# Kernel tuning notes

Measured on AMD Instinct MI355X. Metric: run time of the kernel, lower is better.

Reference implementation:

```python
import jax, jax.numpy as jnp
import numpy as np

# ---- config (matches init_kwargs) ----
B, N = 2, 192
NCG, L0, L1, ANUM = 16, 16, 8, 2
RAD_MAXR, NB, H = 4.0, 10, 32
SQ2 = 1.4142135623730951

RS0 = {0: NCG}
RS_HID = {0: L0, 1: L1}
RS_FIN = {0: ANUM, 1: ANUM}
LMAX_SH = 2


def relu_r(x):  # rescaled_act.relu: unit second moment under N(0,1)
    return jax.nn.relu(x) * SQ2


def sigmoid_r(x):  # rescaled_act.sigmoid
    return jax.nn.sigmoid(x) * 1.84623


def _cg():
    # Real-basis coupling tensors C[i_out, j_in, m_filter]; l=1 components ordered (y,z,x).
    c000 = np.ones((1, 1, 1))
    eye3 = np.eye(3)
    c101 = (eye3 / np.sqrt(3.0)).reshape(3, 1, 3)
    c011 = (eye3 / np.sqrt(3.0)).reshape(1, 3, 3)
    c110 = (eye3 / np.sqrt(3.0)).reshape(3, 3, 1)
    eps = np.zeros((3, 3, 3))
    for i, j, k in [(0, 1, 2), (1, 2, 0), (2, 0, 1)]:
        eps[i, j, k] = 1.0
        eps[j, i, k] = -1.0
    c111 = eps / np.sqrt(6.0)
    c = 1.0925484305920792
    b = 0.31539156525252005
    d = 0.5462742152960396
    m = np.zeros((3, 3, 5))  # index 0=y, 1=z, 2=x
    m[2, 0, 0] = m[0, 2, 0] = c / 2            # ~ x*y
    m[0, 1, 1] = m[1, 0, 1] = c / 2            # ~ y*z
    m[1, 1, 2] = 2 * b; m[0, 0, 2] = -b; m[2, 2, 2] = -b  # ~ 2z^2-x^2-y^2
    m[2, 1, 3] = m[1, 2, 3] = c / 2            # ~ x*z
    m[2, 2, 4] = d; m[0, 0, 4] = -d            # ~ x^2-y^2
    c112 = m / np.linalg.norm(m)
    return {(0, 0, 0): c000, (1, 0, 1): c101, (0, 1, 1): c011,
            (1, 1, 0): c110, (1, 1, 1): c111, (1, 1, 2): c112}

CG = {k: jnp.asarray(v, jnp.float32) for k, v in _cg().items()}


def paths_for(rs_in, rs_out):
    out = []
    for lo in sorted(rs_out):
        for li in sorted(rs_in):
            for lf in range(abs(lo - li), min(lo + li, LMAX_SH) + 1):
                out.append((lo, li, lf, rs_out[lo], rs_in[li]))
    return out


def total_w(rs_in, rs_out):
    return sum(mo * mi for _, _, _, mo, mi in paths_for(rs_in, rs_out))


def convolution(feat, geo, w0, b0, wout, rs_in, rs_out):
    # feat: dict l -> [B,N,mul,2l+1]; geo: [B,N,3]
    rel = geo[:, :, None, :] - geo[:, None, :, :]              # [B,N,N,3]
    r = jnp.sqrt(jnp.sum(rel * rel, -1) + 1e-12)               # [B,N,N]
    u = rel / jnp.maximum(r, 1e-6)[..., None]
    x_, y_, z_ = u[..., 0], u[..., 1], u[..., 2]
    Y = {0: jnp.full(r.shape + (1,), 0.28209479177387814, r.dtype),
         1: 0.4886025119029199 * jnp.stack([y_, z_, x_], -1),
         2: jnp.stack([1.0925484305920792 * x_ * y_,
                       1.0925484305920792 * y_ * z_,
                       0.31539156525252005 * (2 * z_ * z_ - x_ * x_ - y_ * y_),
                       1.0925484305920792 * x_ * z_,
                       0.5462742152960396 * (x_ * x_ - y_ * y_)], -1)}
    # CosineBasisModel: overlapping cos^2 bumps on [0, RAD_MAXR]
    centers = jnp.linspace(0.0, RAD_MAXR, NB)
    step = RAD_MAXR / (NB - 1)
    dg = (r[..., None] - centers) / step
    basis = jnp.where(jnp.abs(dg) < 1.0, jnp.cos(0.5 * jnp.pi * dg) ** 2, 0.0)
    h = relu_r(basis @ (w0 / np.sqrt(NB)) + b0)                # [B,N,N,H]
    Rw = h @ (wout / np.sqrt(H))                               # [B,N,N,total_w]

    plist = paths_for(rs_in, rs_out)
    npaths = {lo: sum(1 for p in plist if p[0] == lo) for lo in rs_out}
    out = {lo: jnp.zeros(geo.shape[:2] + (rs_out[lo], 2 * lo + 1), geo.dtype)
           for lo in rs_out}
    off = 0
    for lo, li, lf, mo, mi in plist:
        w = Rw[..., off:off + mo * mi].reshape(Rw.shape[:3] + (mo, mi))
        off += mo * mi
        contrib = jnp.einsum('zabuv,zabm,ijm,zbvj->zaui', w, Y[lf],
                             CG[(lo, li, lf)], feat[li], optimize=True)
        out[lo] = out[lo] + contrib / np.sqrt(mi * npaths[lo])
    return out


def gated_block(feat, geo, w0, b0, wout, rs_in, rs_out):
    n_gates = sum(m for l, m in rs_out.items() if l > 0)
    rs_conv = dict(rs_out)
    rs_conv[0] = rs_out.get(0, 0) + n_gates
    c = convolution(feat, geo, w0, b0, wout, rs_in, rs_conv)
    m0 = rs_out.get(0, 0)
    out = {0: relu_r(c[0][:, :, :m0])}
    gates = sigmoid_r(c[0][:, :, m0:])                         # [B,N,n_gates,1]
    g_off = 0
    for l in sorted(rs_out):
        if l == 0:
            continue
        ml = rs_out[l]
        out[l] = c[l] * gates[:, :, g_off:g_off + ml]
        g_off += ml
    return out


def _forward(features, geometry, c0_w0, c0_b0, c0_wout, c1_w0, c1_b0, c1_wout,
             c2_w0, c2_b0, c2_wout):
    s = 1.0 / np.sqrt(N)  # output.div(geometry.size(1)**0.5) before every layer
    f = {0: features[..., None] * s}
    f = gated_block(f, geometry, c0_w0, c0_b0, c0_wout, RS0, RS_HID)
    f = {l: v * s for l, v in f.items()}
    f = gated_block(f, geometry, c1_w0, c1_b0, c1_wout, RS_HID, RS_HID)
    f = {l: v * s for l, v in f.items()}
    f = convolution(f, geometry, c2_w0, c2_b0, c2_wout, RS_HID, RS_FIN)
    # final Rs = [(1,0),(1,1)] * atomic_nums -> interleave scalar+vector per species
    out = jnp.concatenate([f[0], f[1]], axis=-1)               # [B,N,ANUM,4]
    return out.reshape(B, N, ANUM * 4)


def setup_inputs() -> dict:
    key = jax.random.key(0)
    ks = jax.random.split(key, 8)
    RS_G = {0: L0 + L1, 1: L1}  # gated conv output: scalars + gates, then l=1
    return {
        'features': jax.random.normal(ks[0], (B, N, NCG), jnp.float32),
        'geometry': jax.random.normal(ks[1], (B, N, 3), jnp.float32),
        'c0_w0': jax.random.normal(ks[2], (NB, H), jnp.float32),
        'c0_b0': jnp.zeros((H,), jnp.float32),
        'c0_wout': jax.random.normal(ks[3], (H, total_w(RS0, RS_G)), jnp.float32),
        'c1_w0': jax.random.normal(ks[4], (NB, H), jnp.float32),
        'c1_b0': jnp.zeros((H,), jnp.float32),
        'c1_wout': jax.random.normal(ks[5], (H, total_w(RS_HID, RS_G)), jnp.float32),
        'c2_w0': jax.random.normal(ks[6], (NB, H), jnp.float32),
        'c2_b0': jnp.zeros((H,), jnp.float32),
        'c2_wout': jax.random.normal(ks[7], (H, total_w(RS_HID, RS_FIN)), jnp.float32),
    }


def reference(features, geometry, c0_w0, c0_b0, c0_wout, c1_w0, c1_b0, c1_wout,
              c2_w0, c2_b0, c2_wout):
    return _forward(features, geometry, c0_w0, c0_b0, c0_wout,
                    c1_w0, c1_b0, c1_wout, c2_w0, c2_b0, c2_wout)
```

## Files before the change

### kernel.cpp

```cpp
#include <hip/hip_runtime.h>
#include <math.h>


#define NN 192
#define BB 2
#define SPLIT 8
#define NS 24
#define NBASIS 10
#define HHID 32

__device__ __forceinline__ float relu_r(float x) {
    return fmaxf(x, 0.0f) * 1.4142135623730951f;
}
__device__ __forceinline__ float sigmoid_r(float x) {
    return (1.0f / (1.0f + expf(-x))) * 1.84623f;
}
__device__ __forceinline__ float dot4(float4 a, float4 b) {
    return a.x * b.x + a.y * b.y + a.z * b.z + a.w * b.w;
}

#define S_SCALE 0.07216878364870323f
#define ISQ10   0.31622776601683794f
#define I32     0.1767766952966369f

__global__ __launch_bounds__(256) void tfn_act(
    const float* __restrict__ part, float* __restrict__ fa0, float* __restrict__ fa1)
{
    int t = blockIdx.x * 256 + threadIdx.x;
    if (t >= BB * NN * 40) return;
    int atom = t / 40, c = t - atom * 40;
    const float* p = &part[atom * SPLIT * 48];
    if (c < 16) {
        float s = 0.0f;
#pragma unroll
        for (int sp = 0; sp < SPLIT; ++sp) s += p[sp * 48 + c];
        fa0[atom * 16 + c] = relu_r(s) * S_SCALE;
    } else {
        int j = c - 16, u = j & 7;
        float g = 0.0f, v = 0.0f;
#pragma unroll
        for (int sp = 0; sp < SPLIT; ++sp) {
            g += p[sp * 48 + 16 + u];
            v += p[sp * 48 + 24 + j];
        }
        fa1[atom * 24 + j] = v * sigmoid_r(g) * S_SCALE;
    }
}

template <int LAYER>
__global__ __launch_bounds__(256, 4) void tfn_s1(
    const float* __restrict__ fin0,
    const float* __restrict__ fin1,
    const float* __restrict__ geo,
    const float* __restrict__ w0g,
    const float* __restrict__ b0g,
    const float* __restrict__ wout,
    float* __restrict__ part)
{
    constexpr int TC    = (LAYER == 0) ? 64 : 144;
    constexpr int TSTR  = (LAYER == 0) ? 64 : 168;
    constexpr int TW    = (LAYER == 0) ? 512 : (LAYER == 1 ? 896 : 128);
    constexpr int NOUT  = (LAYER == 2) ? 8 : 48;
    constexpr int MSTRE = (LAYER == 0) ? 68 : 148;
    constexpr int R     = (LAYER == 0) ? 2 : 4;
    constexpr int C     = (LAYER == 0) ? 4 : 5;

    constexpr int oT   = 0;
    constexpr int oF0  = oT + NS * TSTR;
    constexpr int oF1  = oF0 + NS * 16;
    constexpr int oY   = oF1 + ((LAYER == 0) ? 0 : NS * 24);
    constexpr int oBas = oY + NS * 8;
    constexpr int oH   = oBas + NS * NBASIS;
    constexpr int SM0  = oH + NS * HHID;
    constexpr int oU   = 32 * MSTRE;
    constexpr int SMe  = oU + NOUT * 33;
    constexpr int SM   = (SM0 > SMe) ? SM0 : SMe;
    __shared__ float sm[SM];

    const int tid  = threadIdx.x;
    const int blk  = blockIdx.x;
    const int sp   = blk & (SPLIT - 1);
    const int atom = blk >> 3;
    const int z    = atom / NN, a = atom % NN;
    const int nb0  = sp * NS;

    if constexpr (LAYER == 0) {
        for (int i = tid; i < NS * 16; i += 256)
            sm[oF0 + i] = fin0[(z * NN + nb0) * 16 + i] * S_SCALE;
    } else {
        for (int i = tid; i < NS * 16; i += 256)
            sm[oF0 + i] = fin0[(z * NN + nb0) * 16 + i];
        for (int i = tid; i < NS * 24; i += 256)
            sm[oF1 + i] = fin1[(z * NN + nb0) * 24 + i];
    }
    {
        const float ax = geo[(z * NN + a) * 3 + 0];
        const float ay = geo[(z * NN + a) * 3 + 1];
        const float az = geo[(z * NN + a) * 3 + 2];
        for (int idx = tid; idx < NS * 12; idx += 256) {
            int bl = idx / 12, it = idx - bl * 12;
            const float* gb = &geo[(z * NN + nb0 + bl) * 3];
            float rx = ax - gb[0], ry = ay - gb[1], rz = az - gb[2];
            float r = sqrtf(rx * rx + ry * ry + rz * rz + 1e-12f);
            if (it < NBASIS) {
                float dg = r * 2.25f - (float)it;
                float bas = 0.0f;
                if (fabsf(dg) < 1.0f) {
                    float cc = cosf(1.5707963267948966f * dg);
                    bas = cc * cc;
                }
                sm[oBas + bl * NBASIS + it] = bas;
            } else {
                float inv = 1.0f / fmaxf(r, 1e-6f);
                float ux = rx * inv, uy = ry * inv, uz = rz * inv;
                if (it == 10) {
                    sm[oY + bl * 8 + 0] = 0.4886025119029199f * uy;
                    sm[oY + bl * 8 + 1] = 0.4886025119029199f * uz;
                    sm[oY + bl * 8 + 2] = 0.4886025119029199f * ux;
                } else {
                    sm[oY + bl * 8 + 3] = 1.0925484305920792f * ux * uy;
                    sm[oY + bl * 8 + 4] = 1.0925484305920792f * uy * uz;
                    sm[oY + bl * 8 + 5] = 0.31539156525252005f * (2.0f * uz * uz - ux * ux - uy * uy);
                    sm[oY + bl * 8 + 6] = 1.0925484305920792f * ux * uz;
                    sm[oY + bl * 8 + 7] = 0.5462742152960396f * (ux * ux - uy * uy);
                }
            }
        }
    }
    __syncthreads();

    for (int idx = tid; idx < NS * 32; idx += 256) {
        int bl = idx >> 5, j = idx & 31;
        float su = 0.0f;
#pragma unroll
        for (int k = 0; k < NBASIS; ++k)
            su += sm[oBas + bl * NBASIS + k] * w0g[k * HHID + j];
        sm[oH + idx] = relu_r(su * ISQ10 + b0g[j]);
    }
    if constexpr (LAYER == 0) {
        for (int idx = tid; idx < NS * 16; idx += 256) {
            int loc = idx >> 4, c = idx & 15;
            sm[oT + loc * TSTR + c] = 0.28209479177387814f * sm[oF0 + loc * 16 + c];
        }
#pragma unroll
        for (int i2 = 0; i2 < 3; ++i2)
            for (int idx = tid; idx < NS * 16; idx += 256) {
                int loc = idx >> 4, v = idx & 15;
                sm[oT + loc * TSTR + 16 + i2 * 16 + v] =
                    sm[oY + loc * 8 + i2] * sm[oF0 + loc * 16 + v] * 0.5773502691896258f;
            }
    } else {
        for (int idx = tid; idx < NS * 16; idx += 256) {
            int loc = idx >> 4, c = idx & 15;
            sm[oT + loc * TSTR + c] = 0.28209479177387814f * sm[oF0 + loc * 16 + c];
        }
        for (int idx = tid; idx < NS * 8; idx += 256) {
            int loc = idx >> 3, u = idx & 7;
            const float* Yb = &sm[oY + loc * 8];
            const float* fT = &sm[oF1 + loc * 24];
            sm[oT + loc * TSTR + 16 + u] =
                (fT[u] * Yb[0] + fT[8 + u] * Yb[1] + fT[16 + u] * Yb[2]) * 0.5773502691896258f;
        }
#pragma unroll
        for (int i2 = 0; i2 < 3; ++i2)
            for (int idx = tid; idx < NS * 16; idx += 256) {
                int loc = idx >> 4, v = idx & 15;
                sm[oT + loc * TSTR + 24 + i2 * 16 + v] =
                    sm[oY + loc * 8 + i2] * sm[oF0 + loc * 16 + v] * 0.5773502691896258f;
            }
        for (int idx = tid; idx < NS * 24; idx += 256) {
            int loc = idx / 24, j = idx - loc * 24;
            sm[oT + loc * TSTR + 72 + j] =
                sm[oF1 + loc * 24 + j] * (0.28209479177387814f * 0.5773502691896258f);
        }
#pragma unroll
        for (int i2 = 0; i2 < 3; ++i2) {
            const int i1 = (i2 + 1) % 3, i3 = (i2 + 2) % 3;
            for (int idx = tid; idx < NS * 8; idx += 256) {
                int loc = idx >> 3, u = idx & 7;
                const float* Yb = &sm[oY + loc * 8];
                const float* fT = &sm[oF1 + loc * 24];
                sm[oT + loc * TSTR + 96 + i2 * 8 + u] =
                    (fT[i1 * 8 + u] * Yb[i3] - fT[i3 * 8 + u] * Yb[i1]) * 0.4082482904638631f;
            }
        }
#pragma unroll
        for (int i2 = 0; i2 < 3; ++i2)
            for (int idx = tid; idx < NS * 8; idx += 256) {
                int loc = idx >> 3, u = idx & 7;
                const float* Yb = &sm[oY + loc * 8];
                const float* fT = &sm[oF1 + loc * 24];
                const float D  = 0.31622776601683794f;
                const float Bc = 0.18257418583505536f;
                float f0v = fT[u], f1v = fT[8 + u], f2v = fT[16 + u];
                float Y20 = Yb[3], Y21 = Yb[4], Y22 = Yb[5], Y23 = Yb[6], Y24 = Yb[7];
                float val;
                if (i2 == 0)      val = D * (Y20 * f2v + Y21 * f1v) - (Bc * Y22 + D * Y24) * f0v;
                else if (i2 == 1) val = D * (Y21 * f0v + Y23 * f2v) + 2.0f * Bc * Y22 * f1v;
                else              val = D * (Y20 * f0v + Y23 * f1v + Y24 * f2v) - Bc * Y22 * f2v;
                sm[oT + loc * TSTR + 120 + i2 * 8 + u] = val;
            }
    }
    __syncthreads();

    float acc[R][C];
#pragma unroll
    for (int rr = 0; rr < R; ++rr)
#pragma unroll
        for (int cc = 0; cc < C; ++cc) acc[rr][cc] = 0.0f;

    if constexpr (LAYER == 0) {
        const int hr = tid >> 4, cg = tid & 15;
#pragma unroll 4
        for (int bl = 0; bl < NS; ++bl) {
            float2 hv = *(const float2*)&sm[oH + bl * 32 + hr * 2];
            float4 tv = *(const float4*)&sm[oT + bl * 64 + cg * 4];
            float hvv[2] = {hv.x, hv.y};
            float tvv[4] = {tv.x, tv.y, tv.z, tv.w};
#pragma unroll
            for (int rr = 0; rr < 2; ++rr)
#pragma unroll
                for (int cc = 0; cc < 4; ++cc) acc[rr][cc] += hvv[rr] * tvv[cc];
        }
    } else {
        const int hr = tid >> 5, cg = tid & 31;
#pragma unroll 4
        for (int bl = 0; bl < NS; ++bl) {
            float4 hv = *(const float4*)&sm[oH + bl * 32 + hr * 4];
            const float* tp = &sm[oT + bl * TSTR + cg * 5];
            float hvv[4] = {hv.x, hv.y, hv.z, hv.w};
            float t0 = tp[0], t1 = tp[1], t2 = tp[2], t3 = tp[3], t4 = tp[4];
#pragma unroll
            for (int rr = 0; rr < 4; ++rr) {
                acc[rr][0] += hvv[rr] * t0;
                acc[rr][1] += hvv[rr] * t1;
                acc[rr][2] += hvv[rr] * t2;
                acc[rr][3] += hvv[rr] * t3;
                acc[rr][4] += hvv[rr] * t4;
            }
        }
    }
    __syncthreads();

    {
        const int hr = (LAYER == 0) ? (tid >> 4) : (tid >> 5);
        const int cg = (LAYER == 0) ? (tid & 15) : (tid & 31);
#pragma unroll
        for (int rr = 0; rr < R; ++rr)
#pragma unroll
            for (int cc = 0; cc < C; ++cc) {
                int col = cg * C + cc;
                if (col < TC) sm[(hr * R + rr) * MSTRE + col] = acc[rr][cc];
            }
    }
    __syncthreads();

    constexpr int NITEM = NOUT * 32;
    for (int rp = 0; rp < NITEM / 256; ++rp) {
        int idx = rp * 256 + tid;
        int h = idx / NOUT, o = idx - h * NOUT;
        const float* wr = &wout[h * TW];
        const float* mr = &sm[h * MSTRE];
        float U;
        if constexpr (LAYER == 0) {
            const float sc = I32 * 0.25f;
            float accv;
            if (o < 24) {
                const float4* w4 = (const float4*)(wr + o * 16);
                const float4* m4 = (const float4*)(mr);
                accv = dot4(w4[0], m4[0]) + dot4(w4[1], m4[1])
                     + dot4(w4[2], m4[2]) + dot4(w4[3], m4[3]);
            } else {
                int j = o - 24, u = j & 7, i2 = j >> 3;
                const float4* w4 = (const float4*)(wr + 384 + u * 16);
                const float4* m4 = (const float4*)(mr + 16 + i2 * 16);
                accv = dot4(w4[0], m4[0]) + dot4(w4[1], m4[1])
                     + dot4(w4[2], m4[2]) + dot4(w4[3], m4[3]);
            }
            U = accv * sc;
        } else if constexpr (LAYER == 1) {
            float aA, aB;
            if (o < 24) {
                const float4* w4 = (const float4*)(wr + o * 16);
                const float4* m4 = (const float4*)(mr);
                aA = dot4(w4[0], m4[0]) + dot4(w4[1], m4[1])
                   + dot4(w4[2], m4[2]) + dot4(w4[3], m4[3]);
                const float4* w8 = (const float4*)(wr + 384 + o * 8);
                const float4* m8 = (const float4*)(mr + 16);
                aB = dot4(w8[0], m8[0]) + dot4(w8[1], m8[1]);
                U = (aA * I32 + aB * 0.25f) * I32;
            } else {
                int j = o - 24, u = j & 7, i2 = j >> 3;
                const float4* w4 = (const float4*)(wr + 576 + u * 16);
                const float4* m4 = (const float4*)(mr + 24 + i2 * 16);
                aA = dot4(w4[0], m4[0]) + dot4(w4[1], m4[1])
                   + dot4(w4[2], m4[2]) + dot4(w4[3], m4[3]);
                const float4* wB0 = (const float4*)(wr + 704 + u * 8);
                const float4* wB1 = (const float4*)(wr + 768 + u * 8);
                const float4* wB2 = (const float4*)(wr + 832 + u * 8);
                const float4* mB0 = (const float4*)(mr + 72 + i2 * 8);
                const float4* mB1 = (const float4*)(mr + 96 + i2 * 8);
                const float4* mB2 = (const float4*)(mr + 120 + i2 * 8);
                aB = dot4(wB0[0], mB0[0]) + dot4(wB0[1], mB0[1])
                   + dot4(wB1[0], mB1[0]) + dot4(wB1[1], mB1[1])
                   + dot4(wB2[0], mB2[0]) + dot4(wB2[1], mB2[1]);
                U = (aA * 0.125f + aB * I32) * I32;
            }
        } else {
            float aA, aB;
            if (o < 2) {
                const float4* w4 = (const float4*)(wr + o * 16);
                const float4* m4 = (const float4*)(mr);
                aA = dot4(w4[0], m4[0]) + dot4(w4[1], m4[1])
                   + dot4(w4[2], m4[2]) + dot4(w4[3], m4[3]);
                const float4* w8 = (const float4*)(wr + 32 + o * 8);
                const float4* m8 = (const float4*)(mr + 16);
                aB = dot4(w8[0], m8[0]) + dot4(w8[1], m8[1]);
                U = (aA * I32 + aB * 0.25f) * I32;
            } else {
                int j = o - 2, u = j & 1, i2 = j >> 1;
                const float4* w4 = (const float4*)(wr + 48 + u * 16);
                const float4* m4 = (const float4*)(mr + 24 + i2 * 16);
                aA = dot4(w4[0], m4[0]) + dot4(w4[1], m4[1])
                   + dot4(w4[2], m4[2]) + dot4(w4[3], m4[3]);
                const float4* wB0 = (const float4*)(wr + 80 + u * 8);
                const float4* wB1 = (const float4*)(wr + 96 + u * 8);
                const float4* wB2 = (const float4*)(wr + 112 + u * 8);
                const float4* mB0 = (const float4*)(mr + 72 + i2 * 8);
                const float4* mB1 = (const float4*)(mr + 96 + i2 * 8);
                const float4* mB2 = (const float4*)(mr + 120 + i2 * 8);
                aB = dot4(wB0[0], mB0[0]) + dot4(wB0[1], mB0[1])
                   + dot4(wB1[0], mB1[0]) + dot4(wB1[1], mB1[1])
                   + dot4(wB2[0], mB2[0]) + dot4(wB2[1], mB2[1]);
                U = (aA * 0.125f + aB * I32) * I32;
            }
        }
        sm[oU + o * 33 + h] = U;
    }
    __syncthreads();

    if (tid < NOUT) {
        float su = 0.0f;
#pragma unroll
        for (int h = 0; h < 32; ++h) su += sm[oU + tid * 33 + h];
        part[blk * NOUT + tid] = su;
    }
}

__global__ __launch_bounds__(256) void tfn_fin(
    const float* __restrict__ part2, float* __restrict__ out)
{
    int t = blockIdx.x * 256 + threadIdx.x;
    int atom = t >> 3, o = t & 7;
    const float* p = &part2[atom * SPLIT * 8];
    float su = ((p[o] + p[8 + o]) + (p[16 + o] + p[24 + o]))
             + ((p[32 + o] + p[40 + o]) + (p[48 + o] + p[56 + o]));
    int pos;
    if (o < 2) pos = o * 4;
    else { int j = o - 2; int i2 = j >> 1, u = j & 1; pos = u * 4 + 1 + i2; }
    out[atom * 8 + pos] = su;
}

template <int LAYER>
__global__ __launch_bounds__(256) void tfn_layer_mono(
    const float* __restrict__ geo,
    const float* __restrict__ fin0,
    const float* __restrict__ fin1,
    const float* __restrict__ w0,
    const float* __restrict__ b0g,
    const float* __restrict__ wout,
    float* __restrict__ o0,
    float* __restrict__ o1)
{
    constexpr int TC   = (LAYER == 0) ? 64 : 144;
    constexpr int TW   = (LAYER == 0) ? 512 : (LAYER == 1 ? 896 : 128);
    constexpr int CPT  = TC / 8;
    constexpr int CPTT = TC / 16;

    const int tid = threadIdx.x;
    const int blk = blockIdx.x;
    const int z = blk / NN, a = blk % NN;

    __shared__ float geoL[NN * 3];
    __shared__ float f0L[NN * 16];
    __shared__ float f1L[(LAYER == 0) ? 1 : (NN * 24)];
    __shared__ float w0L[NBASIS * HHID];
    __shared__ float b0L[HHID];
    __shared__ float YC[16 * 8];
    __shared__ float basC[16 * NBASIS];
    __shared__ float hC[16 * HHID];
    __shared__ float tC[16 * TC];
    __shared__ float Mlds[HHID * TC];
    __shared__ float outS[32];

    const float s = S_SCALE;

    for (int i = tid; i < NN * 3; i += 256) geoL[i] = geo[z * NN * 3 + i];
    for (int i = tid; i < NN * 16; i += 256) {
        float v = fin0[z * NN * 16 + i];
        if (LAYER == 0) v *= s;
        f0L[i] = v;
    }
    if constexpr (LAYER != 0) {
        for (int i = tid; i < NN * 24; i += 256) f1L[i] = fin1[z * NN * 24 + i];
    }
    for (int i = tid; i < NBASIS * HHID; i += 256) w0L[i] = w0[i];
    if (tid < HHID) b0L[tid] = b0g[tid];
    __syncthreads();

    const float ax = geoL[a * 3 + 0], ay = geoL[a * 3 + 1], az = geoL[a * 3 + 2];

    float Macc[CPT];
#pragma unroll
    for (int j = 0; j < CPT; ++j) Macc[j] = 0.0f;
    const int hh  = tid >> 3;
    const int cg0 = (tid & 7) * CPT;

    for (int cb = 0; cb < NN / 16; ++cb) {
        {
            const int bl = tid & 15, item = tid >> 4;
            const int b = cb * 16 + bl;
            float rx = ax - geoL[b * 3 + 0];
            float ry = ay - geoL[b * 3 + 1];
            float rz = az - geoL[b * 3 + 2];
            float r = sqrtf(rx * rx + ry * ry + rz * rz + 1e-12f);
            float inv = 1.0f / fmaxf(r, 1e-6f);
            float ux = rx * inv, uy = ry * inv, uz = rz * inv;
            if (item < NBASIS) {
                float dg = r * 2.25f - (float)item;
                float bas = 0.0f;
                if (fabsf(dg) < 1.0f) {
                    float cc = cosf(1.5707963267948966f * dg);
                    bas = cc * cc;
                }
                basC[bl * NBASIS + item] = bas;
            } else if (item == 10) {
                YC[bl * 8 + 0] = 0.4886025119029199f * uy;
                YC[bl * 8 + 1] = 0.4886025119029199f * uz;
                YC[bl * 8 + 2] = 0.4886025119029199f * ux;
            } else if (item == 11) {
                YC[bl * 8 + 3] = 1.0925484305920792f * ux * uy;
                YC[bl * 8 + 4] = 1.0925484305920792f * uy * uz;
                YC[bl * 8 + 5] = 0.31539156525252005f * (2.0f * uz * uz - ux * ux - uy * uy);
                YC[bl * 8 + 6] = 1.0925484305920792f * ux * uz;
                YC[bl * 8 + 7] = 0.5462742152960396f * (ux * ux - uy * uy);
            }
        }
        __syncthreads();

#pragma unroll
        for (int rep = 0; rep < 2; ++rep) {
            int idx = tid + rep * 256;
            int bl = idx >> 5, h2 = idx & 31;
            float su = 0.0f;
#pragma unroll
            for (int k = 0; k < NBASIS; ++k) su += basC[bl * NBASIS + k] * w0L[k * HHID + h2];
            hC[bl * HHID + h2] = relu_r(su * ISQ10 + b0L[h2]);
        }

        {
            const int bl = tid >> 4, cg = tid & 15;
            const int b = cb * 16 + bl;
            const float* Yb = &YC[bl * 8];
#pragma unroll
            for (int jj = 0; jj < CPTT; ++jj) {
                int c = cg * CPTT + jj;
                float val;
                if constexpr (LAYER == 0) {
                    if (c < 16) {
                        val = 0.28209479177387814f * f0L[b * 16 + c];
                    } else {
                        int q = c - 16, v = q / 3, i2 = q % 3;
                        val = Yb[i2] * f0L[b * 16 + v] * 0.5773502691896258f;
                    }
                } else {
                    if (c < 16) {
                        val = 0.28209479177387814f * f0L[b * 16 + c];
                    } else if (c < 24) {
                        int v = c - 16;
                        const float* f = &f1L[(b * 8 + v) * 3];
                        val = (f[0] * Yb[0] + f[1] * Yb[1] + f[2] * Yb[2]) * 0.5773502691896258f;
                    } else if (c < 72) {
                        int q = c - 24, v = q / 3, i2 = q % 3;
                        val = Yb[i2] * f0L[b * 16 + v] * 0.5773502691896258f;
                    } else if (c < 96) {
                        int q = c - 72, v = q / 3, i2 = q % 3;
                        val = f1L[(b * 8 + v) * 3 + i2] * (0.28209479177387814f * 0.5773502691896258f);
                    } else if (c < 120) {
                        int q = c - 96, v = q / 3, i2 = q % 3;
                        const float* f = &f1L[(b * 8 + v) * 3];
                        int i1 = (i2 + 1) % 3, i3 = (i2 + 2) % 3;
                        val = (f[i1] * Yb[i3] - f[i3] * Yb[i1]) * 0.4082482904638631f;
                    } else {
                        int q = c - 120, v = q / 3, i2 = q % 3;
                        const float* f = &f1L[(b * 8 + v) * 3];
                        const float D = 0.31622776601683794f;
                        const float Bc = 0.18257418583505536f;
                        float Y20 = Yb[3], Y21 = Yb[4], Y22 = Yb[5], Y23 = Yb[6], Y24 = Yb[7];
                        if (i2 == 0)      val = D * (Y20 * f[2] + Y21 * f[1]) - (Bc * Y22 + D * Y24) * f[0];
                        else if (i2 == 1) val = D * (Y21 * f[0] + Y23 * f[2]) + 2.0f * Bc * Y22 * f[1];
                        else              val = D * (Y20 * f[0] + Y23 * f[1] + Y24 * f[2]) - Bc * Y22 * f[2];
                    }
                }
                tC[bl * TC + c] = val;
            }
        }
        __syncthreads();

#pragma unroll 4
        for (int bl = 0; bl < 16; ++bl) {
            float hv = hC[bl * HHID + hh];
#pragma unroll
            for (int j = 0; j < CPT; ++j) Macc[j] += hv * tC[bl * TC + cg0 + j];
        }
        __syncthreads();
    }

#pragma unroll
    for (int j = 0; j < CPT; ++j) Mlds[hh * TC + cg0 + j] = Macc[j];
    __syncthreads();

    const float i32 = I32;

    if constexpr (LAYER == 0) {
        const float sc = i32 * 0.25f;
        float o1v = 0.0f;
        if (tid < 24) {
            float acc = 0.0f;
            for (int h2 = 0; h2 < 32; ++h2) {
                const float* wr = &wout[h2 * TW + tid * 16];
                const float* mr = &Mlds[h2 * TC];
#pragma unroll
                for (int v = 0; v < 16; ++v) acc += wr[v] * mr[v];
            }
            outS[tid] = acc * sc;
        } else if (tid >= 32 && tid < 56) {
            int idx = tid - 32, u = idx / 3, i2 = idx % 3;
            float acc = 0.0f;
            for (int h2 = 0; h2 < 32; ++h2) {
                const float* wr = &wout[h2 * TW + 384 + u * 16];
                const float* mr = &Mlds[h2 * TC + 16 + i2];
#pragma unroll
                for (int v = 0; v < 16; ++v) acc += wr[v] * mr[v * 3];
            }
            o1v = acc * sc;
        }
        __syncthreads();
        if (tid < 16) {
            o0[(z * NN + a) * 16 + tid] = relu_r(outS[tid]) * s;
        } else if (tid >= 32 && tid < 56) {
            int idx = tid - 32, u = idx / 3, i2 = idx % 3;
            float g = sigmoid_r(outS[16 + u]);
            o1[((z * NN + a) * 8 + u) * 3 + i2] = o1v * g * s;
        }
    } else if constexpr (LAYER == 1) {
        float o1v = 0.0f;
        if (tid < 24) {
            float aA = 0.0f, aB = 0.0f;
            for (int h2 = 0; h2 < 32; ++h2) {
                const float* wr = &wout[h2 * TW];
                const float* mr = &Mlds[h2 * TC];
#pragma unroll
                for (int v = 0; v < 16; ++v) aA += wr[tid * 16 + v] * mr[v];
#pragma unroll
                for (int v = 0; v < 8; ++v) aB += wr[384 + tid * 8 + v] * mr[16 + v];
            }
            outS[tid] = (aA * i32 + aB * 0.25f) * i32;
        } else if (tid >= 32 && tid < 56) {
            int idx = tid - 32, u = idx / 3, i2 = idx % 3;
            float aA = 0.0f, aB = 0.0f;
            for (int h2 = 0; h2 < 32; ++h2) {
                const float* wr = &wout[h2 * TW];
                const float* mr = &Mlds[h2 * TC];
#pragma unroll
                for (int v = 0; v < 16; ++v) aA += wr[576 + u * 16 + v] * mr[24 + v * 3 + i2];
#pragma unroll
                for (int v = 0; v < 8; ++v)
                    aB += wr[704 + u * 8 + v] * mr[72 + v * 3 + i2]
                        + wr[768 + u * 8 + v] * mr[96 + v * 3 + i2]
                        + wr[832 + u * 8 + v] * mr[120 + v * 3 + i2];
            }
            o1v = (aA * 0.125f + aB * i32) * i32;
        }
        __syncthreads();
        if (tid < 16) {
            o0[(z * NN + a) * 16 + tid] = relu_r(outS[tid]) * s;
        } else if (tid >= 32 && tid < 56) {
            int idx = tid - 32, u = idx / 3, i2 = idx % 3;
            float g = sigmoid_r(outS[16 + u]);
            o1[((z * NN + a) * 8 + u) * 3 + i2] = o1v * g * s;
        }
    } else {
        if (tid < 2) {
            float aA = 0.0f, aB = 0.0f;
            for (int h2 = 0; h2 < 32; ++h2) {
                const float* wr = &wout[h2 * TW];
                const float* mr = &Mlds[h2 * TC];
#pragma unroll
                for (int v = 0; v < 16; ++v) aA += wr[tid * 16 + v] * mr[v];
#pragma unroll
                for (int v = 0; v < 8; ++v) aB += wr[32 + tid * 8 + v] * mr[16 + v];
            }
            o0[(z * NN + a) * 8 + tid * 4] = (aA * i32 + aB * 0.25f) * i32;
        } else if (tid >= 32 && tid < 38) {
            int idx = tid - 32, u = idx / 3, i2 = idx % 3;
            float aA = 0.0f, aB = 0.0f;
            for (int h2 = 0; h2 < 32; ++h2) {
                const float* wr = &wout[h2 * TW];
                const float* mr = &Mlds[h2 * TC];
#pragma unroll
                for (int v = 0; v < 16; ++v) aA += wr[48 + u * 16 + v] * mr[24 + v * 3 + i2];
#pragma unroll
                for (int v = 0; v < 8; ++v)
                    aB += wr[80 + u * 8 + v] * mr[72 + v * 3 + i2]
                        + wr[96 + u * 8 + v] * mr[96 + v * 3 + i2]
                        + wr[112 + u * 8 + v] * mr[120 + v * 3 + i2];
            }
            o0[(z * NN + a) * 8 + u * 4 + 1 + i2] = (aA * 0.125f + aB * i32) * i32;
        }
    }
}

extern "C" void kernel_launch(void* const* d_in, const int* in_sizes, int n_in,
                              void* d_out, int out_size, void* d_ws, size_t ws_size,
                              hipStream_t stream) {
    const float* features = (const float*)d_in[0];
    const float* geometry = (const float*)d_in[1];
    const float* c0w0   = (const float*)d_in[2];
    const float* c0b0   = (const float*)d_in[3];
    const float* c0wout = (const float*)d_in[4];
    const float* c1w0   = (const float*)d_in[5];
    const float* c1b0   = (const float*)d_in[6];
    const float* c1wout = (const float*)d_in[7];
    const float* c2w0   = (const float*)d_in[8];
    const float* c2b0   = (const float*)d_in[9];
    const float* c2wout = (const float*)d_in[10];
    float* out = (float*)d_out;

    float* ws = (float*)d_ws;
    const size_t NBLK  = (size_t)BB * NN * SPLIT;
    const size_t NATOM = (size_t)BB * NN;
    const size_t need  = NBLK * 48 * 2 + NBLK * 8 + NATOM * 40 * 2;

    if (ws_size >= need * sizeof(float)) {
        float* partA = ws;
        float* partB = partA + NBLK * 48;
        float* part2 = partB + NBLK * 48;
        float* fa0A  = part2 + NBLK * 8;
        float* fa1A  = fa0A + NATOM * 16;
        float* fa0B  = fa1A + NATOM * 24;
        float* fa1B  = fa0B + NATOM * 16;

        dim3 g1((unsigned)NBLK), blk(256);
        dim3 gact((unsigned)((NATOM * 40 + 255) / 256));
        hipLaunchKernelGGL((tfn_s1<0>), g1, blk, 0, stream,
                           features, nullptr, geometry, c0w0, c0b0, c0wout, partA);
        hipLaunchKernelGGL(tfn_act, gact, blk, 0, stream, partA, fa0A, fa1A);
        hipLaunchKernelGGL((tfn_s1<1>), g1, blk, 0, stream,
                           fa0A, fa1A, geometry, c1w0, c1b0, c1wout, partB);
        hipLaunchKernelGGL(tfn_act, gact, blk, 0, stream, partB, fa0B, fa1B);
        hipLaunchKernelGGL((tfn_s1<2>), g1, blk, 0, stream,
                           fa0B, fa1B, geometry, c2w0, c2b0, c2wout, part2);
        hipLaunchKernelGGL(tfn_fin, dim3(BB * NN * 8 / 256), blk, 0, stream,
                           part2, out);
    } else {
        float* f0a = ws;
        float* f1a = f0a + BB * NN * 16;
        float* f0b = f1a + BB * NN * 24;
        float* f1b = f0b + BB * NN * 16;
        dim3 grid(BB * NN), blk(256);
        hipLaunchKernelGGL((tfn_layer_mono<0>), grid, blk, 0, stream,
                           geometry, features, nullptr, c0w0, c0b0, c0wout, f0a, f1a);
        hipLaunchKernelGGL((tfn_layer_mono<1>), grid, blk, 0, stream,
                           geometry, f0a, f1a, c1w0, c1b0, c1wout, f0b, f1b);
        hipLaunchKernelGGL((tfn_layer_mono<2>), grid, blk, 0, stream,
                           geometry, f0b, f1b, c2w0, c2b0, c2wout, out, nullptr);
    }
}
```

Before: 110.9 us.

## Reduce split partial M matrices before applying wout in a per-atom mid kernel

The neighbour-split kernel no longer contracts its partial 32xTC M matrix with wout. It writes the raw partial M to workspace, and a new per-atom kernel sums the SPLIT partials, does the wout contraction once per atom and applies the gate/activation (or the final output permutation). This cuts the wout contraction work by a factor of SPLIT and merges the activation and final kernels into the mid kernel. In exchange, each split block now writes a much larger partial (32x144 floats instead of 48), which adds global memory traffic, and the per-atom mid kernel runs on only 384 blocks.

```diff
diff --git a/kernel.cpp b/kernel.cpp
--- a/kernel.cpp
+++ b/kernel.cpp
@@ -23,30 +23,6 @@
 #define ISQ10   0.31622776601683794f
 #define I32     0.1767766952966369f
 
-__global__ __launch_bounds__(256) void tfn_act(
-    const float* __restrict__ part, float* __restrict__ fa0, float* __restrict__ fa1)
-{
-    int t = blockIdx.x * 256 + threadIdx.x;
-    if (t >= BB * NN * 40) return;
-    int atom = t / 40, c = t - atom * 40;
-    const float* p = &part[atom * SPLIT * 48];
-    if (c < 16) {
-        float s = 0.0f;
-#pragma unroll
-        for (int sp = 0; sp < SPLIT; ++sp) s += p[sp * 48 + c];
-        fa0[atom * 16 + c] = relu_r(s) * S_SCALE;
-    } else {
-        int j = c - 16, u = j & 7;
-        float g = 0.0f, v = 0.0f;
-#pragma unroll
-        for (int sp = 0; sp < SPLIT; ++sp) {
-            g += p[sp * 48 + 16 + u];
-            v += p[sp * 48 + 24 + j];
-        }
-        fa1[atom * 24 + j] = v * sigmoid_r(g) * S_SCALE;
-    }
-}
-
 template <int LAYER>
 __global__ __launch_bounds__(256, 4) void tfn_s1(
     const float* __restrict__ fin0,
@@ -54,14 +30,10 @@
     const float* __restrict__ geo,
     const float* __restrict__ w0g,
     const float* __restrict__ b0g,
-    const float* __restrict__ wout,
-    float* __restrict__ part)
+    float* __restrict__ Mpart)
 {
     constexpr int TC    = (LAYER == 0) ? 64 : 144;
     constexpr int TSTR  = (LAYER == 0) ? 64 : 168;
-    constexpr int TW    = (LAYER == 0) ? 512 : (LAYER == 1 ? 896 : 128);
-    constexpr int NOUT  = (LAYER == 2) ? 8 : 48;
-    constexpr int MSTRE = (LAYER == 0) ? 68 : 148;
     constexpr int R     = (LAYER == 0) ? 2 : 4;
     constexpr int C     = (LAYER == 0) ? 4 : 5;
 
@@ -71,10 +43,7 @@
     constexpr int oY   = oF1 + ((LAYER == 0) ? 0 : NS * 24);
     constexpr int oBas = oY + NS * 8;
     constexpr int oH   = oBas + NS * NBASIS;
-    constexpr int SM0  = oH + NS * HHID;
-    constexpr int oU   = 32 * MSTRE;
-    constexpr int SMe  = oU + NOUT * 33;
-    constexpr int SM   = (SM0 > SMe) ? SM0 : SMe;
+    constexpr int SM   = oH + NS * HHID;
     __shared__ float sm[SM];
 
     const int tid  = threadIdx.x;
@@ -222,6 +191,12 @@
 #pragma unroll
                 for (int cc = 0; cc < 4; ++cc) acc[rr][cc] += hvv[rr] * tvv[cc];
         }
+        float* mp = &Mpart[(size_t)blk * (32 * TC)];
+#pragma unroll
+        for (int rr = 0; rr < 2; ++rr)
+#pragma unroll
+            for (int cc = 0; cc < 4; ++cc)
+                mp[(hr * 2 + rr) * TC + cg * 4 + cc] = acc[rr][cc];
     } else {
         const int hr = tid >> 5, cg = tid & 31;
 #pragma unroll 4
@@ -239,25 +214,51 @@
                 acc[rr][4] += hvv[rr] * t4;
             }
         }
+        float* mp = &Mpart[(size_t)blk * (32 * TC)];
+#pragma unroll
+        for (int rr = 0; rr < 4; ++rr)
+#pragma unroll
+            for (int cc = 0; cc < 5; ++cc) {
+                int col = cg * 5 + cc;
+                if (col < TC) mp[(hr * 4 + rr) * TC + col] = acc[rr][cc];
+            }
+    }
+}
+
+template <int LAYER>
+__global__ __launch_bounds__(256) void tfn_mid(
+    const float* __restrict__ Mpart,
+    const float* __restrict__ wout,
+    float* __restrict__ o0,
+    float* __restrict__ o1)
+{
+    constexpr int TC    = (LAYER == 0) ? 64 : 144;
+    constexpr int TW    = (LAYER == 0) ? 512 : (LAYER == 1 ? 896 : 128);
+    constexpr int NOUT  = (LAYER == 2) ? 8 : 48;
+    constexpr int MSTRE = (LAYER == 0) ? 68 : 148;
+    constexpr int MTOT  = 32 * TC;
+
+    constexpr int oU = 32 * MSTRE;
+    constexpr int oP = oU + NOUT * 33;
+    __shared__ float sm[oP + NOUT];
+
+    const int tid  = threadIdx.x;
+    const int atom = blockIdx.x;
+    const float* base = &Mpart[(size_t)atom * SPLIT * MTOT];
+
+    for (int idx = tid; idx < MTOT / 4; idx += 256) {
+        int e = idx * 4, row = e / TC, col = e - row * TC;
+        float4 s4 = make_float4(0.f, 0.f, 0.f, 0.f);
+#pragma unroll
+        for (int sp = 0; sp < SPLIT; ++sp) {
+            float4 v = *(const float4*)&base[sp * MTOT + e];
+            s4.x += v.x; s4.y += v.y; s4.z += v.z; s4.w += v.w;
+        }
+        *(float4*)&sm[row * MSTRE + col] = s4;
     }
     __syncthreads();
 
-    {
-        const int hr = (LAYER == 0) ? (tid >> 4) : (tid >> 5);
-        const int cg = (LAYER == 0) ? (tid & 15) : (tid & 31);
-#pragma unroll
-        for (int rr = 0; rr < R; ++rr)
-#pragma unroll
-            for (int cc = 0; cc < C; ++cc) {
-                int col = cg * C + cc;
-                if (col < TC) sm[(hr * R + rr) * MSTRE + col] = acc[rr][cc];
-            }
-    }
-    __syncthreads();
-
-    constexpr int NITEM = NOUT * 32;
-    for (int rp = 0; rp < NITEM / 256; ++rp) {
-        int idx = rp * 256 + tid;
+    for (int idx = tid; idx < NOUT * 32; idx += 256) {
         int h = idx / NOUT, o = idx - h * NOUT;
         const float* wr = &wout[h * TW];
         const float* mr = &sm[h * MSTRE];
@@ -343,22 +344,28 @@
         float su = 0.0f;
 #pragma unroll
         for (int h = 0; h < 32; ++h) su += sm[oU + tid * 33 + h];
-        part[blk * NOUT + tid] = su;
-    }
-}
-
-__global__ __launch_bounds__(256) void tfn_fin(
-    const float* __restrict__ part2, float* __restrict__ out)
-{
-    int t = blockIdx.x * 256 + threadIdx.x;
-    int atom = t >> 3, o = t & 7;
-    const float* p = &part2[atom * SPLIT * 8];
-    float su = ((p[o] + p[8 + o]) + (p[16 + o] + p[24 + o]))
-             + ((p[32 + o] + p[40 + o]) + (p[48 + o] + p[56 + o]));
-    int pos;
-    if (o < 2) pos = o * 4;
-    else { int j = o - 2; int i2 = j >> 1, u = j & 1; pos = u * 4 + 1 + i2; }
-    out[atom * 8 + pos] = su;
+        sm[oP + tid] = su;
+    }
+    __syncthreads();
+
+    if constexpr (LAYER != 2) {
+        if (tid < 40) {
+            if (tid < 16) {
+                o0[atom * 16 + tid] = relu_r(sm[oP + tid]) * S_SCALE;
+            } else {
+                int j = tid - 16;
+                o1[atom * 24 + j] =
+                    sm[oP + 24 + j] * sigmoid_r(sm[oP + 16 + (j & 7)]) * S_SCALE;
+            }
+        }
+    } else {
+        if (tid < 8) {
+            int o = tid, pos;
+            if (o < 2) pos = o * 4;
+            else { int j = o - 2, i2 = j >> 1, u = j & 1; pos = u * 4 + 1 + i2; }
+            o0[atom * 8 + pos] = sm[oP + o];
+        }
+    }
 }
 
 template <int LAYER>
@@ -640,29 +647,26 @@
     float* ws = (float*)d_ws;
     const size_t NBLK  = (size_t)BB * NN * SPLIT;
     const size_t NATOM = (size_t)BB * NN;
-    const size_t need  = NBLK * 48 * 2 + NBLK * 8 + NATOM * 40 * 2;
+    const size_t MT    = (size_t)32 * 144;
+    const size_t need  = NBLK * MT + NATOM * 40 * 2;
 
     if (ws_size >= need * sizeof(float)) {
-        float* partA = ws;
-        float* partB = partA + NBLK * 48;
-        float* part2 = partB + NBLK * 48;
-        float* fa0A  = part2 + NBLK * 8;
+        float* Mpart = ws;
+        float* fa0A  = Mpart + NBLK * MT;
         float* fa1A  = fa0A + NATOM * 16;
         float* fa0B  = fa1A + NATOM * 24;
         float* fa1B  = fa0B + NATOM * 16;
 
-        dim3 g1((unsigned)NBLK), blk(256);
-        dim3 gact((unsigned)((NATOM * 40 + 255) / 256));
+        dim3 g1((unsigned)NBLK), gm((unsigned)NATOM), blk(256);
         hipLaunchKernelGGL((tfn_s1<0>), g1, blk, 0, stream,
-                           features, nullptr, geometry, c0w0, c0b0, c0wout, partA);
-        hipLaunchKernelGGL(tfn_act, gact, blk, 0, stream, partA, fa0A, fa1A);
+                           features, nullptr, geometry, c0w0, c0b0, Mpart);
+        hipLaunchKernelGGL((tfn_mid<0>), gm, blk, 0, stream, Mpart, c0wout, fa0A, fa1A);
         hipLaunchKernelGGL((tfn_s1<1>), g1, blk, 0, stream,
-                           fa0A, fa1A, geometry, c1w0, c1b0, c1wout, partB);
-        hipLaunchKernelGGL(tfn_act, gact, blk, 0, stream, partB, fa0B, fa1B);
+                           fa0A, fa1A, geometry, c1w0, c1b0, Mpart);
+        hipLaunchKernelGGL((tfn_mid<1>), gm, blk, 0, stream, Mpart, c1wout, fa0B, fa1B);
         hipLaunchKernelGGL((tfn_s1<2>), g1, blk, 0, stream,
-                           fa0B, fa1B, geometry, c2w0, c2b0, c2wout, part2);
-        hipLaunchKernelGGL(tfn_fin, dim3(BB * NN * 8 / 256), blk, 0, stream,
-                           part2, out);
+                           fa0B, fa1B, geometry, c2w0, c2b0, Mpart);
+        hipLaunchKernelGGL((tfn_mid<2>), gm, blk, 0, stream, Mpart, c2wout, out, nullptr);
     } else {
         float* f0a = ws;
         float* f1a = f0a + BB * NN * 16;
```

Result: slower. 128.0 us (+15.4%).
